# Optimization experiments

Hardware: AMD Instinct MI355X
Metric: run time of the kernel (lower is better)

## Reference

```python
import jax, jax.numpy as jnp
import numpy as np

NENTITY = 200000
NRELATION = 500
HIDDEN = 256
GAMMA = 12.0
EPS = 2.0
EMB_RANGE = (GAMMA + EPS) / HIDDEN


def setup_inputs() -> dict:
    key = jax.random.key(0)
    ks = jax.random.split(key, 8)
    B, NEG = 256, 1024
    head = jax.random.randint(ks[0], (B, 1), 0, NENTITY)
    tail = jax.random.randint(ks[1], (B, NEG), 0, NENTITY)
    relation = jax.random.randint(ks[2], (B,), 0, NRELATION)
    entity_emb = jax.random.uniform(ks[3], (NENTITY, HIDDEN), jnp.float32, -EMB_RANGE, EMB_RANGE)
    relation_emb = jax.random.uniform(ks[4], (NRELATION, 2 * HIDDEN), jnp.float32, -EMB_RANGE, EMB_RANGE)
    lim = 1.0 / np.sqrt(2 * HIDDEN)
    W_fc = jax.random.uniform(ks[5], (HIDDEN, 2 * HIDDEN), jnp.float32, -lim, lim)
    b_fc = jax.random.uniform(ks[6], (HIDDEN,), jnp.float32, -lim, lim)
    return {"head": head, "tail": tail, "relation": relation,
            "entity_emb": entity_emb, "relation_emb": relation_emb,
            "W_fc": W_fc, "b_fc": b_fc}


def _l2_normalize(x):
    # F.normalize(x, p=2, dim=-1): x / max(||x||_2, 1e-12)
    n = jnp.sqrt(jnp.sum(x * x, axis=-1, keepdims=True))
    return x / jnp.maximum(n, 1e-12)


def reference(head, tail, relation, entity_emb, relation_emb, W_fc, b_fc):
    # gather embeddings
    h = entity_emb[head]                      # [B, 1,   d]
    t = entity_emb[tail]                      # [B, NEG, d]
    r = relation_emb[relation][:, None, :]    # [B, 1, 2d]
    re_head, re_tail = jnp.split(r, 2, axis=-1)   # each [B, 1, d]
    # broadcast relation halves to match head/tail sample counts, then concat
    re_h = jnp.broadcast_to(re_head, h.shape)
    re_t = jnp.broadcast_to(re_tail, t.shape)
    h_cat = jnp.concatenate([h, re_h], axis=-1)   # [B, 1,   2d]
    t_cat = jnp.concatenate([t, re_t], axis=-1)   # [B, NEG, 2d]
    # shared small FC (torch Linear: x @ W^T + b)
    h_fc = jnp.einsum('bnk,dk->bnd', h_cat, W_fc) + b_fc
    t_fc = jnp.einsum('bnk,dk->bnd', t_cat, W_fc) + b_fc
    h_n = _l2_normalize(h_fc)
    t_n = _l2_normalize(t_fc)
    diff = h_n - t_n                              # [B, NEG, d]
    score = GAMMA - jnp.sum(jnp.abs(diff), axis=2)  # [B, NEG]
    return score
```

## Files before the change

kernel.cpp:

```cpp
#include <hip/hip_runtime.h>
#include <math.h>

#define NENTITY 200000
#define HIDDEN 256
#define NEG 1024
#define NBATCH 256
#define GAMMA_F 12.0f
#define BM 32
#define NTILES 8
#define NBLK 1024
#define NT_P 8
#define CHUNK 128

typedef short v8s __attribute__((ext_vector_type(8)));
typedef float v4f __attribute__((ext_vector_type(4)));
typedef unsigned int u32;

#define LDS_BARRIER() asm volatile("s_waitcnt lgkmcnt(0)\n\ts_barrier" ::: "memory")

__device__ __forceinline__ short f2bf(float x) {
    u32 u = __float_as_uint(x);
    u = (u + 0x7fffu + ((u >> 16) & 1u)) >> 16;
    return (short)u;
}

__device__ __forceinline__ u32 rhu(float f) { return __float_as_uint(f) + 0x8000u; }
__device__ __forceinline__ v8s pack8(const float4& x0, const float4& x1) {
    int4 fr;
    fr.x = __builtin_amdgcn_perm(rhu(x0.y), rhu(x0.x), 0x07060302u);
    fr.y = __builtin_amdgcn_perm(rhu(x0.w), rhu(x0.z), 0x07060302u);
    fr.z = __builtin_amdgcn_perm(rhu(x1.y), rhu(x1.x), 0x07060302u);
    fr.w = __builtin_amdgcn_perm(rhu(x1.w), rhu(x1.z), 0x07060302u);
    return __builtin_bit_cast(v8s, fr);
}

__global__ __launch_bounds__(256) void prep_kernel(
    const int* __restrict__ head, const int* __restrict__ relation,
    const float* __restrict__ entity_emb, const float* __restrict__ relation_emb,
    const float* __restrict__ W_fc, const float* __restrict__ b_fc,
    short* __restrict__ W1bf, float* __restrict__ h_n, float* __restrict__ rel_part)
{
    const int b = blockIdx.x;
    const int t = threadIdx.x;

    W1bf[b * HIDDEN + t] = f2bf(W_fc[(size_t)b * 2 * HIDDEN + t]);

    __shared__ float xh[2 * HIDDEN];
    __shared__ float xt[HIDDEN];
    __shared__ float red[256];

    const int hidx = head[b];
    const int r = relation[b];
    xh[t]          = entity_emb[(size_t)hidx * HIDDEN + t];
    xh[HIDDEN + t] = relation_emb[(size_t)r * 2 * HIDDEN + t];
    xt[t]          = relation_emb[(size_t)r * 2 * HIDDEN + HIDDEN + t];
    __syncthreads();

    const float4* wrow = reinterpret_cast<const float4*>(W_fc + (size_t)t * 2 * HIDDEN);
    float hf = b_fc[t];
    float rp = b_fc[t];
    #pragma unroll 4
    for (int kk = 0; kk < HIDDEN / 4; ++kk) {
        float4 w = wrow[kk];
        hf += xh[4*kk+0]*w.x + xh[4*kk+1]*w.y + xh[4*kk+2]*w.z + xh[4*kk+3]*w.w;
    }
    #pragma unroll 4
    for (int kk = 0; kk < HIDDEN / 4; ++kk) {
        float4 w = wrow[HIDDEN/4 + kk];
        hf += xh[HIDDEN+4*kk+0]*w.x + xh[HIDDEN+4*kk+1]*w.y + xh[HIDDEN+4*kk+2]*w.z + xh[HIDDEN+4*kk+3]*w.w;
        rp += xt[4*kk+0]*w.x + xt[4*kk+1]*w.y + xt[4*kk+2]*w.z + xt[4*kk+3]*w.w;
    }
    rel_part[b * HIDDEN + t] = rp;

    red[t] = hf * hf;
    __syncthreads();
    for (int s = 128; s > 0; s >>= 1) {
        if (t < s) red[t] += red[t + s];
        __syncthreads();
    }
    const float norm = sqrtf(red[0]);
    h_n[b * HIDDEN + t] = hf / fmaxf(norm, 1e-12f);
}

__global__ __launch_bounds__(256, 2) void proj_kernel(
    const float* __restrict__ entity_emb, const short* __restrict__ W1bf,
    short* __restrict__ P)
{
    __shared__ __align__(16) float Asf[2][BM * HIDDEN];

    const int t = threadIdx.x;
    const int w = t >> 6;
    const int l = t & 63;
    const int c = t & 15;
    const int g = (t >> 4) & 3;
    const int E0 = blockIdx.x * (NT_P * BM);

    v8s Wf[4][8];
    #pragma unroll
    for (int f = 0; f < 4; ++f) {
        const short* bsrc = W1bf + (size_t)(64 * w + f * 16 + c) * HIDDEN + g * 8;
        #pragma unroll
        for (int kt = 0; kt < 8; ++kt)
            Wf[f][kt] = *reinterpret_cast<const v8s*>(bsrc + kt * 32);
    }
    #pragma unroll
    for (int f = 0; f < 4; ++f)
        #pragma unroll
        for (int kt = 0; kt < 8; ++kt)
            asm volatile("" : "+v"(Wf[f][kt]));

    v4f st[8];
    auto issue = [&](int j) {
        #pragma unroll
        for (int i = 0; i < 8; ++i) {
            int row = E0 + j * BM + w * 8 + i;
            row = row < NENTITY ? row : NENTITY - 1;
            st[i] = *reinterpret_cast<const v4f*>(
                entity_emb + (size_t)row * HIDDEN + (l << 2));
        }
        __builtin_amdgcn_sched_barrier(0);
    };
    auto commit = [&](int buf) {
        #pragma unroll
        for (int i = 0; i < 8; ++i) {
            const int r = w * 8 + i;
            *reinterpret_cast<v4f*>(&Asf[buf][r * HIDDEN + ((l ^ (r & 7)) << 2)]) = st[i];
        }
    };

    issue(0);
    commit(0);
    LDS_BARRIER();

    #pragma unroll 1
    for (int j = 0; j < NT_P; ++j) {
        const int cur = j & 1;
        if (j + 1 < NT_P) issue(j + 1);

        v4f acc[4][2];
        #pragma unroll
        for (int f = 0; f < 4; ++f)
            #pragma unroll
            for (int et = 0; et < 2; ++et)
                acc[f][et] = v4f{0.f, 0.f, 0.f, 0.f};

        const float* a0base = &Asf[cur][c * HIDDEN];
        const float* a1base = &Asf[cur][(16 + c) * HIDDEN];
        const int swz = c & 7;

        #pragma unroll
        for (int kt = 0; kt < 8; ++kt) {
            const int u0 = kt * 8 + g * 2;
            float4 x0 = *reinterpret_cast<const float4*>(a0base + (((u0    ) ^ swz) << 2));
            float4 x1 = *reinterpret_cast<const float4*>(a0base + (((u0 + 1) ^ swz) << 2));
            float4 y0 = *reinterpret_cast<const float4*>(a1base + (((u0    ) ^ swz) << 2));
            float4 y1 = *reinterpret_cast<const float4*>(a1base + (((u0 + 1) ^ swz) << 2));
            v8s e0 = pack8(x0, x1);
            v8s e1 = pack8(y0, y1);
            #pragma unroll
            for (int f = 0; f < 4; ++f) {
                acc[f][0] = __builtin_amdgcn_mfma_f32_16x16x32_bf16(Wf[f][kt], e0, acc[f][0], 0, 0, 0);
                acc[f][1] = __builtin_amdgcn_mfma_f32_16x16x32_bf16(Wf[f][kt], e1, acc[f][1], 0, 0, 0);
            }
        }

        if (j + 1 < NT_P) commit(cur ^ 1);

        #pragma unroll
        for (int et = 0; et < 2; ++et) {
            const int e = E0 + j * BM + et * 16 + c;
            if (e < NENTITY) {
                short* dst = P + (size_t)e * HIDDEN + 64 * w + g * 4;
                #pragma unroll
                for (int f = 0; f < 4; ++f) {
                    uint2 pk;
                    pk.x = __builtin_amdgcn_perm(rhu(acc[f][et][1]), rhu(acc[f][et][0]), 0x07060302u);
                    pk.y = __builtin_amdgcn_perm(rhu(acc[f][et][3]), rhu(acc[f][et][2]), 0x07060302u);
                    *reinterpret_cast<uint2*>(dst + f * 16) = pk;
                }
            }
        }

        LDS_BARRIER();
    }
}

__global__ __launch_bounds__(256) void score2_kernel(
    const int* __restrict__ tail, const short* __restrict__ P,
    const float* __restrict__ h_n, const float* __restrict__ rel_part,
    float* __restrict__ out)
{
    const int t = threadIdx.x;
    const int w = t >> 6;
    const int l = t & 63;
    const int b = blockIdx.x >> 3;
    const int chunk = blockIdx.x & 7;
    const int base = b * NEG + chunk * CHUNK;

    __shared__ int tl[CHUNK];
    if (t < CHUNK) tl[t] = tail[base + t];

    const float4 hh = *reinterpret_cast<const float4*>(h_n + b * HIDDEN + 4 * l);
    const float4 rp = *reinterpret_cast<const float4*>(rel_part + b * HIDDEN + 4 * l);
    __syncthreads();

    uint2 st2[8];
    #pragma unroll
    for (int i = 0; i < 8; ++i)
        st2[i] = *(reinterpret_cast<const uint2*>(P + (size_t)tl[w * 32 + i] * HIDDEN) + l);

    #pragma unroll
    for (int p = 0; p < 32; ++p) {
        uint2 v = st2[p & 7];
        if (p + 8 < 32)
            st2[p & 7] = *(reinterpret_cast<const uint2*>(
                P + (size_t)tl[w * 32 + p + 8] * HIDDEN) + l);

        float t0 = __uint_as_float(v.x << 16)          + rp.x;
        float t1 = __uint_as_float(v.x & 0xffff0000u)  + rp.y;
        float t2 = __uint_as_float(v.y << 16)          + rp.z;
        float t3 = __uint_as_float(v.y & 0xffff0000u)  + rp.w;

        float ssq = t0 * t0 + t1 * t1 + t2 * t2 + t3 * t3;
        #pragma unroll
        for (int mask = 1; mask < 64; mask <<= 1) ssq += __shfl_xor(ssq, mask);
        const float rn = 1.f / fmaxf(sqrtf(ssq), 1e-12f);

        float l1 = fabsf(hh.x - t0 * rn) + fabsf(hh.y - t1 * rn)
                 + fabsf(hh.z - t2 * rn) + fabsf(hh.w - t3 * rn);
        #pragma unroll
        for (int mask = 1; mask < 64; mask <<= 1) l1 += __shfl_xor(l1, mask);

        if (l == 0) out[base + w * 32 + p] = GAMMA_F - l1;
    }
}

__global__ __launch_bounds__(256, 2) void score_kernel(
    const int* __restrict__ tail, const float* __restrict__ entity_emb,
    const short* __restrict__ W1bf, const float* __restrict__ h_n,
    const float* __restrict__ rel_part, float* __restrict__ out)
{
    __shared__ __align__(16) float Asf[2][BM * HIDDEN];
    __shared__ int tails[NTILES * BM];
    __shared__ float ssq_lds[4][BM];
    __shared__ float l1_lds[4][BM];

    const int t = threadIdx.x;
    const int w = t >> 6;
    const int l = t & 63;
    const int c = t & 15;
    const int g = (t >> 4) & 3;
    const int b = blockIdx.x >> 2;

    tails[t] = tail[blockIdx.x * (NTILES * BM) + t];

    float rlv[4], hnv[4];
    #pragma unroll
    for (int ntl = 0; ntl < 4; ++ntl) {
        const int n = 64 * w + ntl * 16 + c;
        rlv[ntl] = rel_part[b * HIDDEN + n];
        hnv[ntl] = h_n[b * HIDDEN + n];
    }

    v8s Bf[4][8];
    #pragma unroll
    for (int ntl = 0; ntl < 4; ++ntl) {
        const short* bsrc = W1bf + (size_t)(64 * w + ntl * 16 + c) * HIDDEN + g * 8;
        #pragma unroll
        for (int kt = 0; kt < 8; ++kt)
            Bf[ntl][kt] = *reinterpret_cast<const v8s*>(bsrc + kt * 32);
    }

    __syncthreads();

    v4f st[8];
    auto issue = [&](int j) {
        #pragma unroll
        for (int i = 0; i < 8; ++i) {
            const int r = w * 8 + i;
            const float* src = entity_emb + (size_t)tails[j * BM + r] * HIDDEN + (l << 2);
            st[i] = *reinterpret_cast<const v4f*>(src);
        }
        __builtin_amdgcn_sched_barrier(0);
    };
    auto commit = [&](int buf) {
        #pragma unroll
        for (int i = 0; i < 8; ++i) {
            const int r = w * 8 + i;
            *reinterpret_cast<v4f*>(&Asf[buf][r * HIDDEN + ((l ^ (r & 7)) << 2)]) = st[i];
        }
    };

    issue(0);
    commit(0);
    LDS_BARRIER();

    #pragma unroll 1
    for (int j = 0; j < NTILES; ++j) {
        const int cur = j & 1;
        if (j + 1 < NTILES) issue(j + 1);

        v4f acc[2][4];
        #pragma unroll
        for (int mt = 0; mt < 2; ++mt)
            #pragma unroll
            for (int ntl = 0; ntl < 4; ++ntl)
                acc[mt][ntl] = v4f{0.f, 0.f, 0.f, 0.f};

        const float* a0base = &Asf[cur][c * HIDDEN];
        const float* a1base = &Asf[cur][(16 + c) * HIDDEN];
        const int swz = c & 7;

        #pragma unroll
        for (int kt = 0; kt < 8; ++kt) {
            const int u0 = kt * 8 + g * 2;
            float4 x0 = *reinterpret_cast<const float4*>(a0base + (((u0    ) ^ swz) << 2));
            float4 x1 = *reinterpret_cast<const float4*>(a0base + (((u0 + 1) ^ swz) << 2));
            float4 y0 = *reinterpret_cast<const float4*>(a1base + (((u0    ) ^ swz) << 2));
            float4 y1 = *reinterpret_cast<const float4*>(a1base + (((u0 + 1) ^ swz) << 2));
            v8s a0 = pack8(x0, x1);
            v8s a1 = pack8(y0, y1);
            #pragma unroll
            for (int ntl = 0; ntl < 4; ++ntl) {
                acc[0][ntl] = __builtin_amdgcn_mfma_f32_16x16x32_bf16(a0, Bf[ntl][kt], acc[0][ntl], 0, 0, 0);
                acc[1][ntl] = __builtin_amdgcn_mfma_f32_16x16x32_bf16(a1, Bf[ntl][kt], acc[1][ntl], 0, 0, 0);
            }
        }

        #pragma unroll
        for (int mt = 0; mt < 2; ++mt) {
            float ssq[4] = {0.f, 0.f, 0.f, 0.f};
            #pragma unroll
            for (int ntl = 0; ntl < 4; ++ntl) {
                #pragma unroll
                for (int r = 0; r < 4; ++r) {
                    float tf = acc[mt][ntl][r] + rlv[ntl];
                    acc[mt][ntl][r] = tf;
                    ssq[r] += tf * tf;
                }
            }
            #pragma unroll
            for (int mask = 1; mask < 16; mask <<= 1) {
                #pragma unroll
                for (int r = 0; r < 4; ++r) ssq[r] += __shfl_xor(ssq[r], mask);
            }
            if (c == 0) {
                #pragma unroll
                for (int r = 0; r < 4; ++r) ssq_lds[w][mt * 16 + g * 4 + r] = ssq[r];
            }
        }
        LDS_BARRIER();

        #pragma unroll
        for (int mt = 0; mt < 2; ++mt) {
            float rn[4], s1[4] = {0.f, 0.f, 0.f, 0.f};
            #pragma unroll
            for (int r = 0; r < 4; ++r) {
                const int m = mt * 16 + g * 4 + r;
                float tot = ssq_lds[0][m] + ssq_lds[1][m] + ssq_lds[2][m] + ssq_lds[3][m];
                rn[r] = 1.f / fmaxf(sqrtf(tot), 1e-12f);
            }
            #pragma unroll
            for (int ntl = 0; ntl < 4; ++ntl) {
                #pragma unroll
                for (int r = 0; r < 4; ++r)
                    s1[r] += fabsf(hnv[ntl] - acc[mt][ntl][r] * rn[r]);
            }
            #pragma unroll
            for (int mask = 1; mask < 16; mask <<= 1) {
                #pragma unroll
                for (int r = 0; r < 4; ++r) s1[r] += __shfl_xor(s1[r], mask);
            }
            if (c == 0) {
                #pragma unroll
                for (int r = 0; r < 4; ++r) l1_lds[w][mt * 16 + g * 4 + r] = s1[r];
            }
        }

        if (j + 1 < NTILES) commit(cur ^ 1);
        LDS_BARRIER();

        if (t < BM) {
            out[blockIdx.x * (NTILES * BM) + j * BM + t] = GAMMA_F -
                (l1_lds[0][t] + l1_lds[1][t] + l1_lds[2][t] + l1_lds[3][t]);
        }
    }
}

extern "C" void kernel_launch(void* const* d_in, const int* in_sizes, int n_in,
                              void* d_out, int out_size, void* d_ws, size_t ws_size,
                              hipStream_t stream)
{
    const int*   head         = (const int*)d_in[0];
    const int*   tail         = (const int*)d_in[1];
    const int*   relation     = (const int*)d_in[2];
    const float* entity_emb   = (const float*)d_in[3];
    const float* relation_emb = (const float*)d_in[4];
    const float* W_fc         = (const float*)d_in[5];
    const float* b_fc         = (const float*)d_in[6];
    float* out = (float*)d_out;

    short* W1bf     = (short*)d_ws;
    float* h_n      = (float*)((char*)d_ws + 131072);
    float* rel_part = (float*)((char*)d_ws + 131072 + 262144);

    prep_kernel<<<NBATCH, 256, 0, stream>>>(head, relation, entity_emb, relation_emb,
                                            W_fc, b_fc, W1bf, h_n, rel_part);

    const size_t P_OFF   = 1ull << 20;
    const size_t P_BYTES = (size_t)NENTITY * HIDDEN * sizeof(short);
    if (ws_size >= P_OFF + P_BYTES) {
        short* P = (short*)((char*)d_ws + P_OFF);
        const int grid = (NENTITY + NT_P * BM - 1) / (NT_P * BM);
        proj_kernel<<<grid, 256, 0, stream>>>(entity_emb, W1bf, P);
        score2_kernel<<<NBATCH * 8, 256, 0, stream>>>(tail, P, h_n, rel_part, out);
    } else {
        score_kernel<<<NBLK, 256, 0, stream>>>(tail, entity_emb, W1bf,
                                               h_n, rel_part, out);
    }
}
```

Baseline: 390.5 us.

## Store bf16 tiles in LDS and split projection across eight waves per block

The projection kernel now converts entity rows to bf16 once when writing them to shared memory, instead of keeping fp32 in LDS and repacking on every MFMA read. This halves the LDS footprint and read traffic. The block grows to 512 threads, so each wave owns 32 output columns instead of 64, which halves the per-wave W fragments, accumulators and staging registers and should allow more resident waves. The trade-off is more waves contending for LDS and barriers, plus a new XOR swizzle on the bf16 layout that must stay free of bank conflicts.

Measured after the change: 396.8 us. Within noise of the previous version (+1.6%).

```diff
diff --git a/kernel.cpp b/kernel.cpp
--- a/kernel.cpp
+++ b/kernel.cpp
@@ -33,6 +33,12 @@
     fr.w = __builtin_amdgcn_perm(rhu(x1.w), rhu(x1.z), 0x07060302u);
     return __builtin_bit_cast(v8s, fr);
 }
+__device__ __forceinline__ uint2 pack4(const v4f& a) {
+    uint2 pk;
+    pk.x = __builtin_amdgcn_perm(rhu(a[1]), rhu(a[0]), 0x07060302u);
+    pk.y = __builtin_amdgcn_perm(rhu(a[3]), rhu(a[2]), 0x07060302u);
+    return pk;
+}
 
 __global__ __launch_bounds__(256) void prep_kernel(
     const int* __restrict__ head, const int* __restrict__ relation,
@@ -82,11 +88,11 @@
     h_n[b * HIDDEN + t] = hf / fmaxf(norm, 1e-12f);
 }
 
-__global__ __launch_bounds__(256, 2) void proj_kernel(
+__global__ __launch_bounds__(512, 4) void proj_kernel(
     const float* __restrict__ entity_emb, const short* __restrict__ W1bf,
     short* __restrict__ P)
 {
-    __shared__ __align__(16) float Asf[2][BM * HIDDEN];
+    __shared__ __align__(16) short Abf[2][BM * HIDDEN];
 
     const int t = threadIdx.x;
     const int w = t >> 6;
@@ -95,25 +101,25 @@
     const int g = (t >> 4) & 3;
     const int E0 = blockIdx.x * (NT_P * BM);
 
-    v8s Wf[4][8];
-    #pragma unroll
-    for (int f = 0; f < 4; ++f) {
-        const short* bsrc = W1bf + (size_t)(64 * w + f * 16 + c) * HIDDEN + g * 8;
+    v8s Wf[2][8];
+    #pragma unroll
+    for (int f2 = 0; f2 < 2; ++f2) {
+        const short* bsrc = W1bf + (size_t)(w * 32 + f2 * 16 + c) * HIDDEN + g * 8;
         #pragma unroll
         for (int kt = 0; kt < 8; ++kt)
-            Wf[f][kt] = *reinterpret_cast<const v8s*>(bsrc + kt * 32);
-    }
-    #pragma unroll
-    for (int f = 0; f < 4; ++f)
+            Wf[f2][kt] = *reinterpret_cast<const v8s*>(bsrc + kt * 32);
+    }
+    #pragma unroll
+    for (int f2 = 0; f2 < 2; ++f2)
         #pragma unroll
         for (int kt = 0; kt < 8; ++kt)
-            asm volatile("" : "+v"(Wf[f][kt]));
-
-    v4f st[8];
+            asm volatile("" : "+v"(Wf[f2][kt]));
+
+    v4f st[4];
     auto issue = [&](int j) {
         #pragma unroll
-        for (int i = 0; i < 8; ++i) {
-            int row = E0 + j * BM + w * 8 + i;
+        for (int i = 0; i < 4; ++i) {
+            int row = E0 + j * BM + w * 4 + i;
             row = row < NENTITY ? row : NENTITY - 1;
             st[i] = *reinterpret_cast<const v4f*>(
                 entity_emb + (size_t)row * HIDDEN + (l << 2));
@@ -121,10 +127,13 @@
         __builtin_amdgcn_sched_barrier(0);
     };
     auto commit = [&](int buf) {
-        #pragma unroll
-        for (int i = 0; i < 8; ++i) {
-            const int r = w * 8 + i;
-            *reinterpret_cast<v4f*>(&Asf[buf][r * HIDDEN + ((l ^ (r & 7)) << 2)]) = st[i];
+        char* base = reinterpret_cast<char*>(&Abf[buf][0]);
+        #pragma unroll
+        for (int i = 0; i < 4; ++i) {
+            const int r = w * 4 + i;
+            uint2 pk = pack4(st[i]);
+            *reinterpret_cast<uint2*>(base + r * 512
+                + (((l >> 1) ^ (r & 7)) << 4) + ((l & 1) << 3)) = pk;
         }
     };
 
@@ -137,30 +146,25 @@
         const int cur = j & 1;
         if (j + 1 < NT_P) issue(j + 1);
 
-        v4f acc[4][2];
-        #pragma unroll
-        for (int f = 0; f < 4; ++f)
-            #pragma unroll
-            for (int et = 0; et < 2; ++et)
-                acc[f][et] = v4f{0.f, 0.f, 0.f, 0.f};
-
-        const float* a0base = &Asf[cur][c * HIDDEN];
-        const float* a1base = &Asf[cur][(16 + c) * HIDDEN];
+        v4f acc[2][2];
+        #pragma unroll
+        for (int et = 0; et < 2; ++et)
+            #pragma unroll
+            for (int f2 = 0; f2 < 2; ++f2)
+                acc[et][f2] = v4f{0.f, 0.f, 0.f, 0.f};
+
+        const char* base = reinterpret_cast<const char*>(&Abf[cur][0]);
         const int swz = c & 7;
 
         #pragma unroll
         for (int kt = 0; kt < 8; ++kt) {
-            const int u0 = kt * 8 + g * 2;
-            float4 x0 = *reinterpret_cast<const float4*>(a0base + (((u0    ) ^ swz) << 2));
-            float4 x1 = *reinterpret_cast<const float4*>(a0base + (((u0 + 1) ^ swz) << 2));
-            float4 y0 = *reinterpret_cast<const float4*>(a1base + (((u0    ) ^ swz) << 2));
-            float4 y1 = *reinterpret_cast<const float4*>(a1base + (((u0 + 1) ^ swz) << 2));
-            v8s e0 = pack8(x0, x1);
-            v8s e1 = pack8(y0, y1);
-            #pragma unroll
-            for (int f = 0; f < 4; ++f) {
-                acc[f][0] = __builtin_amdgcn_mfma_f32_16x16x32_bf16(Wf[f][kt], e0, acc[f][0], 0, 0, 0);
-                acc[f][1] = __builtin_amdgcn_mfma_f32_16x16x32_bf16(Wf[f][kt], e1, acc[f][1], 0, 0, 0);
+            const int u = ((kt * 4 + g) ^ swz) << 4;
+            v8s e0 = *reinterpret_cast<const v8s*>(base + (c)      * 512 + u);
+            v8s e1 = *reinterpret_cast<const v8s*>(base + (16 + c) * 512 + u);
+            #pragma unroll
+            for (int f2 = 0; f2 < 2; ++f2) {
+                acc[0][f2] = __builtin_amdgcn_mfma_f32_16x16x32_bf16(Wf[f2][kt], e0, acc[0][f2], 0, 0, 0);
+                acc[1][f2] = __builtin_amdgcn_mfma_f32_16x16x32_bf16(Wf[f2][kt], e1, acc[1][f2], 0, 0, 0);
             }
         }
 
@@ -170,14 +174,10 @@
         for (int et = 0; et < 2; ++et) {
             const int e = E0 + j * BM + et * 16 + c;
             if (e < NENTITY) {
-                short* dst = P + (size_t)e * HIDDEN + 64 * w + g * 4;
-                #pragma unroll
-                for (int f = 0; f < 4; ++f) {
-                    uint2 pk;
-                    pk.x = __builtin_amdgcn_perm(rhu(acc[f][et][1]), rhu(acc[f][et][0]), 0x07060302u);
-                    pk.y = __builtin_amdgcn_perm(rhu(acc[f][et][3]), rhu(acc[f][et][2]), 0x07060302u);
-                    *reinterpret_cast<uint2*>(dst + f * 16) = pk;
-                }
+                short* dst = P + (size_t)e * HIDDEN + w * 32 + g * 4;
+                #pragma unroll
+                for (int f2 = 0; f2 < 2; ++f2)
+                    *reinterpret_cast<uint2*>(dst + f2 * 16) = pack4(acc[et][f2]);
             }
         }
 
@@ -412,7 +412,7 @@
     if (ws_size >= P_OFF + P_BYTES) {
         short* P = (short*)((char*)d_ws + P_OFF);
         const int grid = (NENTITY + NT_P * BM - 1) / (NT_P * BM);
-        proj_kernel<<<grid, 256, 0, stream>>>(entity_emb, W1bf, P);
+        proj_kernel<<<grid, 512, 0, stream>>>(entity_emb, W1bf, P);
         score2_kernel<<<NBATCH * 8, 256, 0, stream>>>(tail, P, h_n, rel_part, out);
     } else {
         score_kernel<<<NBLK, 256, 0, stream>>>(tail, entity_emb, W1bf,
```
